# Optimization experiments

Measured on AMD Instinct MI355X. Metric: run time of the kernel, lower is better.

The kernel has to match this reference:

```python
import jax, jax.numpy as jnp
import numpy as np

N = 50000       # nodes
E = 800000      # edges (before self-loops)
G = 512         # graphs in batch
IN = 128        # in_channels
HID = 256       # hidden_channels
HEADS = 8
CH = HID // HEADS
NEG_SLOPE = 0.2 # GATConv leaky relu slope
BN_EPS = 1e-5
OUT_CLASSES = [3, 3]


def setup_inputs() -> dict:
    key = jax.random.key(0)
    ks = iter(jax.random.split(key, 64))
    inp = {}
    inp["x"] = jax.random.normal(next(ks), (N, IN), jnp.float32)
    inp["edge_index"] = jax.random.randint(next(ks), (2, E), 0, N)
    inp["batch"] = jnp.sort(jax.random.randint(next(ks), (N,), 0, G))
    dims = [IN, HID, HID]
    for l, d in enumerate(dims, start=1):
        inp[f"W{l}"] = jax.random.normal(next(ks), (d, HID), jnp.float32) / np.float32(np.sqrt(d))
        inp[f"as{l}"] = jax.random.normal(next(ks), (HEADS, CH), jnp.float32) * 0.1
        inp[f"ad{l}"] = jax.random.normal(next(ks), (HEADS, CH), jnp.float32) * 0.1
        inp[f"b{l}"] = jnp.zeros((HID,), jnp.float32)
        inp[f"g{l}"] = 1.0 + 0.1 * jax.random.normal(next(ks), (HID,), jnp.float32)
        inp[f"be{l}"] = 0.1 * jax.random.normal(next(ks), (HID,), jnp.float32)
        inp[f"m{l}"] = 0.1 * jax.random.normal(next(ks), (HID,), jnp.float32)
        inp[f"v{l}"] = 0.5 + jax.random.uniform(next(ks), (HID,), jnp.float32)
    for i, c in enumerate(OUT_CLASSES):
        inp[f"ow{i}"] = jax.random.normal(next(ks), (3 * HID, c), jnp.float32) / np.float32(np.sqrt(3 * HID))
        inp[f"ob{i}"] = jnp.zeros((c,), jnp.float32)
    return inp


def gat_conv(x, W, a_src, a_dst, bias, src, dst):
    # x: [N, D] -> h: [N, H, C]
    h = (x @ W).reshape(N, HEADS, CH)
    s_src = jnp.sum(h * a_src, axis=-1)           # [N, H]
    s_dst = jnp.sum(h * a_dst, axis=-1)           # [N, H]
    alpha = jax.nn.leaky_relu(s_src[src] + s_dst[dst], NEG_SLOPE)  # [E', H]
    # segment softmax over incoming edges of each destination node
    mx = jax.ops.segment_max(alpha, dst, num_segments=N)           # [N, H]
    e = jnp.exp(alpha - mx[dst])
    Z = jax.ops.segment_sum(e, dst, num_segments=N)                # [N, H]
    coef = e / (Z[dst] + 1e-16)                                    # [E', H]
    msg = h[src] * coef[:, :, None]                                # [E', H, C]
    out = jax.ops.segment_sum(msg, dst, num_segments=N)            # [N, H, C]
    return out.reshape(N, HID) + bias


def batch_norm(h, g, b, m, v):
    return (h - m) * jax.lax.rsqrt(v + BN_EPS) * g + b


def reference(x, edge_index, batch,
              W1, as1, ad1, b1, g1, be1, m1, v1,
              W2, as2, ad2, b2, g2, be2, m2, v2,
              W3, as3, ad3, b3, g3, be3, m3, v3,
              ow0, ob0, ow1, ob1):
    # GATConv adds self-loops by default
    loop = jnp.arange(N, dtype=edge_index.dtype)
    src = jnp.concatenate([edge_index[0], loop])
    dst = jnp.concatenate([edge_index[1], loop])

    h = jax.nn.elu(batch_norm(gat_conv(x, W1, as1, ad1, b1, src, dst), g1, be1, m1, v1))
    h = jax.nn.elu(batch_norm(gat_conv(h, W2, as2, ad2, b2, src, dst), g2, be2, m2, v2) + h)
    h = jax.nn.elu(batch_norm(gat_conv(h, W3, as3, ad3, b3, src, dst), g3, be3, m3, v3) + h)

    sums = jax.ops.segment_sum(h, batch, num_segments=G)                       # add pool
    cnt = jax.ops.segment_sum(jnp.ones((N, 1), h.dtype), batch, num_segments=G)
    mean = sums / jnp.maximum(cnt, 1.0)                                        # mean pool
    mx = jax.ops.segment_max(h, batch, num_segments=G)                         # max pool
    mx = jnp.where(jnp.isfinite(mx), mx, 0.0)
    pooled = jnp.concatenate([mean, sums, mx], axis=1)                         # [G, 3*HID]

    return (pooled @ ow0 + ob0, pooled @ ow1 + ob1)
```

## Files before the change

kernel.cpp:

```cpp
#include <hip/hip_runtime.h>
#include <hip/hip_bf16.h>
#include <math.h>

#define N_NODES 50000
#define N_EDGES 800000
#define EP (N_EDGES + N_NODES)
#define G_GRAPHS 512
#define HID 256
#define HEADS 8
#define NEG_SLOPE 0.2f
#define BN_EPS 1e-5f
#define NB_SCAN ((N_NODES + 1023) / 1024)

typedef __attribute__((ext_vector_type(8))) short short8;
typedef __attribute__((ext_vector_type(8))) unsigned short ushort8v;
typedef __attribute__((ext_vector_type(4))) float floatx4;

__device__ __forceinline__ float bf2f(ushort u) {
    return __uint_as_float(((unsigned)u) << 16);
}
__device__ __forceinline__ ushort f2bf(float f) {
    unsigned u = __float_as_uint(f);
    u += 0x7fff + ((u >> 16) & 1);
    return (ushort)(u >> 16);
}


__global__ void hist_kernel(const int* __restrict__ ei, int* __restrict__ fill) {
    int e = blockIdx.x * 256 + threadIdx.x;
    if (e >= EP) return;
    int d = (e < N_EDGES) ? ei[N_EDGES + e] : (e - N_EDGES);
    atomicAdd(&fill[d], 1);
}

__global__ void scan1_kernel(const int* __restrict__ fill, int* __restrict__ rowptr,
                             int* __restrict__ bsum) {
    __shared__ int sdata[1024];
    int tid = threadIdx.x;
    int idx = blockIdx.x * 1024 + tid;
    int v = (idx < N_NODES) ? fill[idx] : 0;
    sdata[tid] = v;
    __syncthreads();
    for (int off = 1; off < 1024; off <<= 1) {
        int x = (tid >= off) ? sdata[tid - off] : 0;
        __syncthreads();
        sdata[tid] += x;
        __syncthreads();
    }
    if (idx < N_NODES) rowptr[idx] = sdata[tid] - v;
    if (tid == 1023) bsum[blockIdx.x] = sdata[1023];
}

__global__ void scan2_kernel(int* __restrict__ bsum) {
    int lane = threadIdx.x;
    int v = (lane < NB_SCAN) ? bsum[lane] : 0;
    int incl = v;
#pragma unroll
    for (int off = 1; off < 64; off <<= 1) {
        int x = __shfl_up(incl, off, 64);
        if (lane >= off) incl += x;
    }
    if (lane < NB_SCAN) bsum[lane] = incl - v;
    if (lane == NB_SCAN - 1) bsum[NB_SCAN] = incl;
}

__global__ void scan3_kernel(int* __restrict__ rowptr, int* __restrict__ fill,
                             const int* __restrict__ bsum) {
    int idx = blockIdx.x * 1024 + threadIdx.x;
    if (idx < N_NODES) {
        int e = rowptr[idx] + bsum[blockIdx.x];
        rowptr[idx] = e;
        fill[idx] = e;
    }
    if (idx == N_NODES) rowptr[N_NODES] = bsum[NB_SCAN];
}

__global__ void scatter_kernel(const int* __restrict__ ei, int* __restrict__ fill,
                               int* __restrict__ esrc) {
    int e = blockIdx.x * 256 + threadIdx.x;
    if (e >= EP) return;
    int s, d;
    if (e < N_EDGES) { s = ei[e]; d = ei[N_EDGES + e]; }
    else             { s = d = e - N_EDGES; }
    int pos = atomicAdd(&fill[d], 1);
    esrc[pos] = s;
}

__global__ void gstart_kernel(const int* __restrict__ batch, int* __restrict__ gstart) {
    int g = blockIdx.x * 64 + threadIdx.x;
    if (g > G_GRAPHS) return;
    int lo = 0, hi = N_NODES;
    while (lo < hi) { int mid = (lo + hi) >> 1; if (batch[mid] < g) lo = mid + 1; else hi = mid; }
    gstart[g] = lo;
}


__global__ void cvt_kernel(const float* __restrict__ in, ushort* __restrict__ out, int n4) {
    int i = blockIdx.x * 256 + threadIdx.x;
    if (i >= n4) return;
    float4 v = *(const float4*)&in[(size_t)i * 4];
    ushort4 o = {f2bf(v.x), f2bf(v.y), f2bf(v.z), f2bf(v.w)};
    *(ushort4*)&out[(size_t)i * 4] = o;
}

__global__ void wt_all_kernel(const float* __restrict__ W0, const float* __restrict__ W1,
                              const float* __restrict__ W2, ushort* __restrict__ Wt0,
                              ushort* __restrict__ Wt1, ushort* __restrict__ Wt2) {
    int m = blockIdx.y;
    const float* W = (m == 0) ? W0 : (m == 1) ? W1 : W2;
    ushort* Wt = (m == 0) ? Wt0 : (m == 1) ? Wt1 : Wt2;
    int K = (m == 0) ? 128 : 256;
    int c = blockIdx.x, k = threadIdx.x;
    if (k < K) Wt[(size_t)c * K + k] = f2bf(W[(size_t)k * HID + c]);
}

#define BM 128
#define BN 128
#define BK 64

__global__ __launch_bounds__(256) void gemm_kernel(
    const ushort* __restrict__ A, const ushort* __restrict__ Bt,
    ushort* __restrict__ C, int M, int K)
{
    __shared__ __align__(16) char As[BM * BK * 2];
    __shared__ __align__(16) char Bs[BN * BK * 2];

    int t = threadIdx.x;
    int w = t >> 6, lane = t & 63;
    int bm = blockIdx.x * BM, bn = blockIdx.y * BN;
    int wr = (w >> 1) * 64, wc = (w & 1) * 64;

    floatx4 acc[4][4] = {};

    int l8 = lane >> 3;
    int cb = ((lane & 7) << 4) ^ ((l8 & 7) << 4);
    int rsw = (lane & 7) << 4;

    for (int k0 = 0; k0 < K; k0 += BK) {
#pragma unroll
        for (int c = 0; c < 4; c++) {
            int q = w * 4 + c;
            int row = q * 8 + l8;
            int ar = bm + row; if (ar > M - 1) ar = M - 1;
            const char* src = (const char*)A + ((size_t)ar * K + k0) * 2 + cb;
            __builtin_amdgcn_global_load_lds(
                (const __attribute__((address_space(1))) void*)src,
                (__attribute__((address_space(3))) void*)&As[q * 1024], 16, 0, 0);
            int br = bn + row;
            const char* srcb = (const char*)Bt + ((size_t)br * K + k0) * 2 + cb;
            __builtin_amdgcn_global_load_lds(
                (const __attribute__((address_space(1))) void*)srcb,
                (__attribute__((address_space(3))) void*)&Bs[q * 1024], 16, 0, 0);
        }
        __syncthreads();

#pragma unroll
        for (int ks = 0; ks < 2; ks++) {
            int kb = ks * 64 + ((lane >> 4) << 4);
            short8 a[4], b[4];
#pragma unroll
            for (int m = 0; m < 4; m++) {
                int row = wr + m * 16 + (lane & 15);
                a[m] = *(const short8*)&As[row * 128 + (kb ^ rsw)];
            }
#pragma unroll
            for (int n = 0; n < 4; n++) {
                int row = wc + n * 16 + (lane & 15);
                b[n] = *(const short8*)&Bs[row * 128 + (kb ^ rsw)];
            }
#pragma unroll
            for (int m = 0; m < 4; m++)
#pragma unroll
                for (int n = 0; n < 4; n++)
                    acc[m][n] = __builtin_amdgcn_mfma_f32_16x16x32_bf16(a[m], b[n], acc[m][n], 0, 0, 0);
        }
        __syncthreads();
    }

    int cl = lane & 15, rh = lane >> 4;
#pragma unroll
    for (int m = 0; m < 4; m++) {
#pragma unroll
        for (int r = 0; r < 4; r++) {
            int row = bm + wr + m * 16 + rh * 4 + r;
            if (row < M) {
                size_t base = (size_t)row * HID + bn + wc;
#pragma unroll
                for (int n = 0; n < 4; n++)
                    C[base + n * 16 + cl] = f2bf(acc[m][n][r]);
            }
        }
    }
}

__global__ void score_kernel(const ushort* __restrict__ hb,
                             const float* __restrict__ asrc,
                             const float* __restrict__ adst,
                             float* __restrict__ ssrc, float* __restrict__ sdst) {
    int idx = blockIdx.x * 256 + threadIdx.x;
    if (idx >= N_NODES * HEADS) return;
    int n = idx >> 3, h = idx & 7;
    const ushort* hp = &hb[(size_t)n * HID + h * 32];
    const float* ap = &asrc[h * 32];
    const float* dp = &adst[h * 32];
    float s1 = 0.f, s2 = 0.f;
#pragma unroll
    for (int j = 0; j < 32; j++) {
        float v = bf2f(hp[j]);
        s1 += v * ap[j];
        s2 += v * dp[j];
    }
    ssrc[idx] = s1;
    sdst[idx] = s2;
}

__global__ __launch_bounds__(256) void agg_kernel(
    const ushort* __restrict__ hb, const float* __restrict__ ssrc,
    const float* __restrict__ sdst, const int* __restrict__ rowptr,
    const int* __restrict__ esrc, const float* __restrict__ bias,
    const float* __restrict__ gam, const float* __restrict__ bet,
    const float* __restrict__ bmean, const float* __restrict__ bvar,
    const float* __restrict__ resid, float* __restrict__ outh,
    ushort* __restrict__ outb) {
    int wid = threadIdx.x >> 6;
    int lane = threadIdx.x & 63;
    int n = blockIdx.x * 4 + wid;
    if (n >= N_NODES) return;
    int start = rowptr[n], end = rowptr[n + 1];
    int slot = lane >> 5;
    int cl = lane & 31;
    int c0 = cl * 8;
    int head = cl >> 2;
    float sdh = ssrc ? sdst[(size_t)n * 8 + head] : 0.f;

    float z = 0.f;
    float acc[8] = {};
    int i = start + slot;
    for (; i + 2 < end; i += 4) {
        int s0 = esrc[i], s1 = esrc[i + 2];
        float a0 = ssrc[(size_t)s0 * 8 + head] + sdh;
        float a1 = ssrc[(size_t)s1 * 8 + head] + sdh;
        a0 = (a0 >= 0.f) ? a0 : NEG_SLOPE * a0;
        a1 = (a1 >= 0.f) ? a1 : NEG_SLOPE * a1;
        float e0 = __expf(a0);
        float e1 = __expf(a1);
        ushort8v h0 = *(const ushort8v*)&hb[(size_t)s0 * HID + c0];
        ushort8v h1 = *(const ushort8v*)&hb[(size_t)s1 * HID + c0];
        z += e0 + e1;
#pragma unroll
        for (int j = 0; j < 8; j++)
            acc[j] += e0 * bf2f(h0[j]) + e1 * bf2f(h1[j]);
    }
    if (i < end) {
        int s = esrc[i];
        float a = ssrc[(size_t)s * 8 + head] + sdh;
        a = (a >= 0.f) ? a : NEG_SLOPE * a;
        float e = __expf(a);
        ushort8v hv = *(const ushort8v*)&hb[(size_t)s * HID + c0];
        z += e;
#pragma unroll
        for (int j = 0; j < 8; j++)
            acc[j] += e * bf2f(hv[j]);
    }
    z += __shfl_xor(z, 32, 64);
#pragma unroll
    for (int j = 0; j < 8; j++)
        acc[j] += __shfl_xor(acc[j], 32, 64);

    if (lane < 32) {
        float inv = 1.f / (z + 1e-16f);
        float4 bv0 = *(const float4*)&bias[c0],   bv1 = *(const float4*)&bias[c0 + 4];
        float4 gv0 = *(const float4*)&gam[c0],    gv1 = *(const float4*)&gam[c0 + 4];
        float4 be0 = *(const float4*)&bet[c0],    be1 = *(const float4*)&bet[c0 + 4];
        float4 mv0 = *(const float4*)&bmean[c0],  mv1 = *(const float4*)&bmean[c0 + 4];
        float4 vv0 = *(const float4*)&bvar[c0],   vv1 = *(const float4*)&bvar[c0 + 4];
        float bs[8] = {bv0.x, bv0.y, bv0.z, bv0.w, bv1.x, bv1.y, bv1.z, bv1.w};
        float gs[8] = {gv0.x, gv0.y, gv0.z, gv0.w, gv1.x, gv1.y, gv1.z, gv1.w};
        float bes[8] = {be0.x, be0.y, be0.z, be0.w, be1.x, be1.y, be1.z, be1.w};
        float ms[8] = {mv0.x, mv0.y, mv0.z, mv0.w, mv1.x, mv1.y, mv1.z, mv1.w};
        float vs[8] = {vv0.x, vv0.y, vv0.z, vv0.w, vv1.x, vv1.y, vv1.z, vv1.w};
        float rs[8] = {};
        if (resid) {
            float4 r0 = *(const float4*)&resid[(size_t)n * HID + c0];
            float4 r1 = *(const float4*)&resid[(size_t)n * HID + c0 + 4];
            rs[0] = r0.x; rs[1] = r0.y; rs[2] = r0.z; rs[3] = r0.w;
            rs[4] = r1.x; rs[5] = r1.y; rs[6] = r1.z; rs[7] = r1.w;
        }
        float out[8];
#pragma unroll
        for (int j = 0; j < 8; j++) {
            float val = acc[j] * inv + bs[j];
            val = (val - ms[j]) * rsqrtf(vs[j] + BN_EPS) * gs[j] + bes[j];
            val += rs[j];
            val = (val > 0.f) ? val : expm1f(val);
            out[j] = val;
        }
        if (outh) {
            float4 o0 = {out[0], out[1], out[2], out[3]};
            float4 o1 = {out[4], out[5], out[6], out[7]};
            *(float4*)&outh[(size_t)n * HID + c0] = o0;
            *(float4*)&outh[(size_t)n * HID + c0 + 4] = o1;
        }
        if (outb) {
            ushort8v ob;
#pragma unroll
            for (int j = 0; j < 8; j++) ob[j] = f2bf(out[j]);
            *(ushort8v*)&outb[(size_t)n * HID + c0] = ob;
        }
    }
}

__global__ void poolhead_kernel(const ushort* __restrict__ hbf, const int* __restrict__ gstart,
                                const float* __restrict__ ow0, const float* __restrict__ ob0,
                                const float* __restrict__ ow1, const float* __restrict__ ob1,
                                float* __restrict__ out) {
    int g = blockIdx.x;
    int t = threadIdx.x;
    int s = gstart[g], e = gstart[g + 1];
    float sum = 0.f, mx = -INFINITY;
    for (int n = s; n < e; n++) {
        float v = bf2f(hbf[(size_t)n * HID + t]);
        sum += v;
        mx = fmaxf(mx, v);
    }
    int cnt = e - s;
    float mean = sum / fmaxf((float)cnt, 1.f);
    if (cnt == 0) mx = 0.f;

    float a0[3], a1[3];
#pragma unroll
    for (int j = 0; j < 3; j++) {
        a0[j] = mean * ow0[t * 3 + j] + sum * ow0[(256 + t) * 3 + j] + mx * ow0[(512 + t) * 3 + j];
        a1[j] = mean * ow1[t * 3 + j] + sum * ow1[(256 + t) * 3 + j] + mx * ow1[(512 + t) * 3 + j];
    }
    __shared__ float sd[6][256];
#pragma unroll
    for (int j = 0; j < 3; j++) { sd[j][t] = a0[j]; sd[3 + j][t] = a1[j]; }
    __syncthreads();
    for (int off = 128; off; off >>= 1) {
        if (t < off) {
#pragma unroll
            for (int j = 0; j < 6; j++) sd[j][t] += sd[j][t + off];
        }
        __syncthreads();
    }
    if (t < 3) {
        out[g * 3 + t] = sd[t][0] + ob0[t];
        out[1536 + g * 3 + t] = sd[3 + t][0] + ob1[t];
    }
}

extern "C" void kernel_launch(void* const* d_in, const int* in_sizes, int n_in,
                              void* d_out, int out_size, void* d_ws, size_t ws_size,
                              hipStream_t stream) {
    const float* x     = (const float*)d_in[0];
    const int*   ei    = (const int*)d_in[1];
    const int*   batch = (const int*)d_in[2];
    const float* W[3]  = {(const float*)d_in[3], (const float*)d_in[11], (const float*)d_in[19]};
    const float* AS[3] = {(const float*)d_in[4], (const float*)d_in[12], (const float*)d_in[20]};
    const float* AD[3] = {(const float*)d_in[5], (const float*)d_in[13], (const float*)d_in[21]};
    const float* B[3]  = {(const float*)d_in[6], (const float*)d_in[14], (const float*)d_in[22]};
    const float* GM[3] = {(const float*)d_in[7], (const float*)d_in[15], (const float*)d_in[23]};
    const float* BE[3] = {(const float*)d_in[8], (const float*)d_in[16], (const float*)d_in[24]};
    const float* M[3]  = {(const float*)d_in[9], (const float*)d_in[17], (const float*)d_in[25]};
    const float* V[3]  = {(const float*)d_in[10], (const float*)d_in[18], (const float*)d_in[26]};
    const float* ow0 = (const float*)d_in[27];
    const float* ob0 = (const float*)d_in[28];
    const float* ow1 = (const float*)d_in[29];
    const float* ob1 = (const float*)d_in[30];
    float* out = (float*)d_out;

    char* p = (char*)d_ws;
    int* rowptr = (int*)p;  p += (size_t)(N_NODES + 1) * 4;
    int* fill   = (int*)p;  p += (size_t)N_NODES * 4;
    int* esrc   = (int*)p;  p += (size_t)EP * 4;
    int* gstart = (int*)p;  p += (size_t)(G_GRAPHS + 1) * 4;
    int* bsum   = (int*)p;  p += (size_t)(NB_SCAN + 1) * 4;
    p = (char*)(((uintptr_t)p + 255) & ~(uintptr_t)255);
    ushort* hb    = (ushort*)p; p += (size_t)N_NODES * HID * 2;
    float*  curh  = (float*)p;  p += (size_t)N_NODES * HID * 4;
    ushort* curhb = (ushort*)p; p += (size_t)N_NODES * HID * 2;
    ushort* xb    = (ushort*)p; p += (size_t)N_NODES * 128 * 2;
    ushort* Wt0   = (ushort*)p; p += (size_t)256 * 128 * 2;
    ushort* Wt1   = (ushort*)p; p += (size_t)256 * 256 * 2;
    ushort* Wt2   = (ushort*)p; p += (size_t)256 * 256 * 2;
    float* ssrc   = (float*)p;  p += (size_t)N_NODES * HEADS * 4;
    float* sdst   = (float*)p;  p += (size_t)N_NODES * HEADS * 4;

    hipMemsetAsync(fill, 0, (size_t)N_NODES * 4, stream);
    hist_kernel<<<(EP + 255) / 256, 256, 0, stream>>>(ei, fill);
    scan1_kernel<<<NB_SCAN, 1024, 0, stream>>>(fill, rowptr, bsum);
    scan2_kernel<<<1, 64, 0, stream>>>(bsum);
    scan3_kernel<<<NB_SCAN, 1024, 0, stream>>>(rowptr, fill, bsum);
    scatter_kernel<<<(EP + 255) / 256, 256, 0, stream>>>(ei, fill, esrc);
    gstart_kernel<<<(G_GRAPHS + 64) / 64, 64, 0, stream>>>(batch, gstart);

    cvt_kernel<<<(N_NODES * 128 / 4 + 255) / 256, 256, 0, stream>>>(x, xb, N_NODES * 128 / 4);
    {
        dim3 wgrid(256, 3);
        wt_all_kernel<<<wgrid, 256, 0, stream>>>(W[0], W[1], W[2], Wt0, Wt1, Wt2);
    }
    const ushort* Wt[3] = {Wt0, Wt1, Wt2};

    dim3 ggrid((N_NODES + BM - 1) / BM, HID / BN);
    int sgrid = (N_NODES * HEADS + 255) / 256;
    int agrid = (N_NODES + 3) / 4;

    gemm_kernel<<<ggrid, 256, 0, stream>>>(xb, Wt[0], hb, N_NODES, 128);
    score_kernel<<<sgrid, 256, 0, stream>>>(hb, AS[0], AD[0], ssrc, sdst);
    agg_kernel<<<agrid, 256, 0, stream>>>(hb, ssrc, sdst, rowptr, esrc,
                                          B[0], GM[0], BE[0], M[0], V[0],
                                          nullptr, curh, curhb);
    gemm_kernel<<<ggrid, 256, 0, stream>>>(curhb, Wt[1], hb, N_NODES, 256);
    score_kernel<<<sgrid, 256, 0, stream>>>(hb, AS[1], AD[1], ssrc, sdst);
    agg_kernel<<<agrid, 256, 0, stream>>>(hb, ssrc, sdst, rowptr, esrc,
                                          B[1], GM[1], BE[1], M[1], V[1],
                                          curh, curh, curhb);
    gemm_kernel<<<ggrid, 256, 0, stream>>>(curhb, Wt[2], hb, N_NODES, 256);
    score_kernel<<<sgrid, 256, 0, stream>>>(hb, AS[2], AD[2], ssrc, sdst);
    agg_kernel<<<agrid, 256, 0, stream>>>(hb, ssrc, sdst, rowptr, esrc,
                                          B[2], GM[2], BE[2], M[2], V[2],
                                          curh, nullptr, curhb);

    poolhead_kernel<<<G_GRAPHS, 256, 0, stream>>>(curhb, gstart, ow0, ob0, ow1, ob1, out);
}
```

Before: 622.2 us.

## Double-buffer GEMM, fuse scan passes, unroll aggregation, keep residual in bf16

The single-block prefix-scan kernel is folded into scan3, so each block recomputes the block offsets itself and one launch goes away. The GEMM now double-buffers its LDS tiles with explicit vmcnt waits and barriers, so the global loads for the next tile overlap the MFMA work on the current one. The aggregation loop handles four edges per slot per iteration to expose more memory-level parallelism. The fp32 residual/activation buffer is dropped: the residual is read from the bf16 copy and updated in place, which cuts aggregation memory traffic but rounds the residual path to bf16.

```diff
diff --git a/kernel.cpp b/kernel.cpp
--- a/kernel.cpp
+++ b/kernel.cpp
@@ -51,28 +51,29 @@
     if (tid == 1023) bsum[blockIdx.x] = sdata[1023];
 }
 
-__global__ void scan2_kernel(int* __restrict__ bsum) {
-    int lane = threadIdx.x;
-    int v = (lane < NB_SCAN) ? bsum[lane] : 0;
-    int incl = v;
-#pragma unroll
-    for (int off = 1; off < 64; off <<= 1) {
-        int x = __shfl_up(incl, off, 64);
-        if (lane >= off) incl += x;
-    }
-    if (lane < NB_SCAN) bsum[lane] = incl - v;
-    if (lane == NB_SCAN - 1) bsum[NB_SCAN] = incl;
-}
-
 __global__ void scan3_kernel(int* __restrict__ rowptr, int* __restrict__ fill,
                              const int* __restrict__ bsum) {
-    int idx = blockIdx.x * 1024 + threadIdx.x;
+    __shared__ int soff[2];
+    int tid = threadIdx.x;
+    if (tid < 64) {
+        int v = (tid < NB_SCAN) ? bsum[tid] : 0;
+        int incl = v;
+#pragma unroll
+        for (int off = 1; off < 64; off <<= 1) {
+            int x = __shfl_up(incl, off, 64);
+            if (tid >= off) incl += x;
+        }
+        if (tid == blockIdx.x) soff[0] = incl - v;
+        if (tid == NB_SCAN - 1) soff[1] = incl;
+    }
+    __syncthreads();
+    int idx = blockIdx.x * 1024 + tid;
     if (idx < N_NODES) {
-        int e = rowptr[idx] + bsum[blockIdx.x];
+        int e = rowptr[idx] + soff[0];
         rowptr[idx] = e;
         fill[idx] = e;
     }
-    if (idx == N_NODES) rowptr[N_NODES] = bsum[NB_SCAN];
+    if (idx == N_NODES) rowptr[N_NODES] = soff[1];
 }
 
 __global__ void scatter_kernel(const int* __restrict__ ei, int* __restrict__ fill,
@@ -122,8 +123,8 @@
     const ushort* __restrict__ A, const ushort* __restrict__ Bt,
     ushort* __restrict__ C, int M, int K)
 {
-    __shared__ __align__(16) char As[BM * BK * 2];
-    __shared__ __align__(16) char Bs[BN * BK * 2];
+    __shared__ __align__(16) char As[2][BM * BK * 2];
+    __shared__ __align__(16) char Bs[2][BN * BK * 2];
 
     int t = threadIdx.x;
     int w = t >> 6, lane = t & 63;
@@ -135,8 +136,9 @@
     int l8 = lane >> 3;
     int cb = ((lane & 7) << 4) ^ ((l8 & 7) << 4);
     int rsw = (lane & 7) << 4;
-
-    for (int k0 = 0; k0 < K; k0 += BK) {
+    int nt = K / BK;
+
+    auto stage = [&](int buf, int k0) {
 #pragma unroll
         for (int c = 0; c < 4; c++) {
             int q = w * 4 + c;
@@ -145,15 +147,31 @@
             const char* src = (const char*)A + ((size_t)ar * K + k0) * 2 + cb;
             __builtin_amdgcn_global_load_lds(
                 (const __attribute__((address_space(1))) void*)src,
-                (__attribute__((address_space(3))) void*)&As[q * 1024], 16, 0, 0);
+                (__attribute__((address_space(3))) void*)&As[buf][q * 1024], 16, 0, 0);
             int br = bn + row;
             const char* srcb = (const char*)Bt + ((size_t)br * K + k0) * 2 + cb;
             __builtin_amdgcn_global_load_lds(
                 (const __attribute__((address_space(1))) void*)srcb,
-                (__attribute__((address_space(3))) void*)&Bs[q * 1024], 16, 0, 0);
-        }
-        __syncthreads();
-
+                (__attribute__((address_space(3))) void*)&Bs[buf][q * 1024], 16, 0, 0);
+        }
+    };
+
+    stage(0, 0);
+    for (int tt = 0; tt < nt; tt++) {
+        int cur = tt & 1;
+        __builtin_amdgcn_s_barrier();
+        if (tt + 1 < nt) {
+            stage(cur ^ 1, (tt + 1) * BK);
+            asm volatile("s_waitcnt vmcnt(8)" ::: "memory");
+        } else {
+            asm volatile("s_waitcnt vmcnt(0)" ::: "memory");
+        }
+        __builtin_amdgcn_sched_barrier(0);
+        __builtin_amdgcn_s_barrier();
+        __builtin_amdgcn_sched_barrier(0);
+
+        const char* asb = As[cur];
+        const char* bsb = Bs[cur];
 #pragma unroll
         for (int ks = 0; ks < 2; ks++) {
             int kb = ks * 64 + ((lane >> 4) << 4);
@@ -161,12 +179,12 @@
 #pragma unroll
             for (int m = 0; m < 4; m++) {
                 int row = wr + m * 16 + (lane & 15);
-                a[m] = *(const short8*)&As[row * 128 + (kb ^ rsw)];
+                a[m] = *(const short8*)&asb[row * 128 + (kb ^ rsw)];
             }
 #pragma unroll
             for (int n = 0; n < 4; n++) {
                 int row = wc + n * 16 + (lane & 15);
-                b[n] = *(const short8*)&Bs[row * 128 + (kb ^ rsw)];
+                b[n] = *(const short8*)&bsb[row * 128 + (kb ^ rsw)];
             }
 #pragma unroll
             for (int m = 0; m < 4; m++)
@@ -174,7 +192,6 @@
                 for (int n = 0; n < 4; n++)
                     acc[m][n] = __builtin_amdgcn_mfma_f32_16x16x32_bf16(a[m], b[n], acc[m][n], 0, 0, 0);
         }
-        __syncthreads();
     }
 
     int cl = lane & 15, rh = lane >> 4;
@@ -220,8 +237,7 @@
     const int* __restrict__ esrc, const float* __restrict__ bias,
     const float* __restrict__ gam, const float* __restrict__ bet,
     const float* __restrict__ bmean, const float* __restrict__ bvar,
-    const float* __restrict__ resid, float* __restrict__ outh,
-    ushort* __restrict__ outb) {
+    const ushort* __restrict__ residb, ushort* __restrict__ outb) {
     int wid = threadIdx.x >> 6;
     int lane = threadIdx.x & 63;
     int n = blockIdx.x * 4 + wid;
@@ -231,27 +247,33 @@
     int cl = lane & 31;
     int c0 = cl * 8;
     int head = cl >> 2;
-    float sdh = ssrc ? sdst[(size_t)n * 8 + head] : 0.f;
+    float sdh = sdst[(size_t)n * 8 + head];
 
     float z = 0.f;
     float acc[8] = {};
     int i = start + slot;
-    for (; i + 2 < end; i += 4) {
-        int s0 = esrc[i], s1 = esrc[i + 2];
+    for (; i + 6 < end; i += 8) {
+        int s0 = esrc[i], s1 = esrc[i + 2], s2 = esrc[i + 4], s3 = esrc[i + 6];
         float a0 = ssrc[(size_t)s0 * 8 + head] + sdh;
         float a1 = ssrc[(size_t)s1 * 8 + head] + sdh;
+        float a2 = ssrc[(size_t)s2 * 8 + head] + sdh;
+        float a3 = ssrc[(size_t)s3 * 8 + head] + sdh;
+        ushort8v h0 = *(const ushort8v*)&hb[(size_t)s0 * HID + c0];
+        ushort8v h1 = *(const ushort8v*)&hb[(size_t)s1 * HID + c0];
+        ushort8v h2 = *(const ushort8v*)&hb[(size_t)s2 * HID + c0];
+        ushort8v h3 = *(const ushort8v*)&hb[(size_t)s3 * HID + c0];
         a0 = (a0 >= 0.f) ? a0 : NEG_SLOPE * a0;
         a1 = (a1 >= 0.f) ? a1 : NEG_SLOPE * a1;
-        float e0 = __expf(a0);
-        float e1 = __expf(a1);
-        ushort8v h0 = *(const ushort8v*)&hb[(size_t)s0 * HID + c0];
-        ushort8v h1 = *(const ushort8v*)&hb[(size_t)s1 * HID + c0];
-        z += e0 + e1;
+        a2 = (a2 >= 0.f) ? a2 : NEG_SLOPE * a2;
+        a3 = (a3 >= 0.f) ? a3 : NEG_SLOPE * a3;
+        float e0 = __expf(a0), e1 = __expf(a1), e2 = __expf(a2), e3 = __expf(a3);
+        z += (e0 + e1) + (e2 + e3);
 #pragma unroll
         for (int j = 0; j < 8; j++)
-            acc[j] += e0 * bf2f(h0[j]) + e1 * bf2f(h1[j]);
-    }
-    if (i < end) {
+            acc[j] += (e0 * bf2f(h0[j]) + e1 * bf2f(h1[j])) +
+                      (e2 * bf2f(h2[j]) + e3 * bf2f(h3[j]));
+    }
+    for (; i < end; i += 2) {
         int s = esrc[i];
         float a = ssrc[(size_t)s * 8 + head] + sdh;
         a = (a >= 0.f) ? a : NEG_SLOPE * a;
@@ -280,33 +302,21 @@
         float ms[8] = {mv0.x, mv0.y, mv0.z, mv0.w, mv1.x, mv1.y, mv1.z, mv1.w};
         float vs[8] = {vv0.x, vv0.y, vv0.z, vv0.w, vv1.x, vv1.y, vv1.z, vv1.w};
         float rs[8] = {};
-        if (resid) {
-            float4 r0 = *(const float4*)&resid[(size_t)n * HID + c0];
-            float4 r1 = *(const float4*)&resid[(size_t)n * HID + c0 + 4];
-            rs[0] = r0.x; rs[1] = r0.y; rs[2] = r0.z; rs[3] = r0.w;
-            rs[4] = r1.x; rs[5] = r1.y; rs[6] = r1.z; rs[7] = r1.w;
-        }
-        float out[8];
+        if (residb) {
+            ushort8v rv = *(const ushort8v*)&residb[(size_t)n * HID + c0];
+#pragma unroll
+            for (int j = 0; j < 8; j++) rs[j] = bf2f(rv[j]);
+        }
+        ushort8v ob;
 #pragma unroll
         for (int j = 0; j < 8; j++) {
             float val = acc[j] * inv + bs[j];
             val = (val - ms[j]) * rsqrtf(vs[j] + BN_EPS) * gs[j] + bes[j];
             val += rs[j];
             val = (val > 0.f) ? val : expm1f(val);
-            out[j] = val;
-        }
-        if (outh) {
-            float4 o0 = {out[0], out[1], out[2], out[3]};
-            float4 o1 = {out[4], out[5], out[6], out[7]};
-            *(float4*)&outh[(size_t)n * HID + c0] = o0;
-            *(float4*)&outh[(size_t)n * HID + c0 + 4] = o1;
-        }
-        if (outb) {
-            ushort8v ob;
-#pragma unroll
-            for (int j = 0; j < 8; j++) ob[j] = f2bf(out[j]);
-            *(ushort8v*)&outb[(size_t)n * HID + c0] = ob;
-        }
+            ob[j] = f2bf(val);
+        }
+        *(ushort8v*)&outb[(size_t)n * HID + c0] = ob;
     }
 }
 
@@ -378,7 +388,6 @@
     int* bsum   = (int*)p;  p += (size_t)(NB_SCAN + 1) * 4;
     p = (char*)(((uintptr_t)p + 255) & ~(uintptr_t)255);
     ushort* hb    = (ushort*)p; p += (size_t)N_NODES * HID * 2;
-    float*  curh  = (float*)p;  p += (size_t)N_NODES * HID * 4;
     ushort* curhb = (ushort*)p; p += (size_t)N_NODES * HID * 2;
     ushort* xb    = (ushort*)p; p += (size_t)N_NODES * 128 * 2;
     ushort* Wt0   = (ushort*)p; p += (size_t)256 * 128 * 2;
@@ -390,7 +399,6 @@
     hipMemsetAsync(fill, 0, (size_t)N_NODES * 4, stream);
     hist_kernel<<<(EP + 255) / 256, 256, 0, stream>>>(ei, fill);
     scan1_kernel<<<NB_SCAN, 1024, 0, stream>>>(fill, rowptr, bsum);
-    scan2_kernel<<<1, 64, 0, stream>>>(bsum);
     scan3_kernel<<<NB_SCAN, 1024, 0, stream>>>(rowptr, fill, bsum);
     scatter_kernel<<<(EP + 255) / 256, 256, 0, stream>>>(ei, fill, esrc);
     gstart_kernel<<<(G_GRAPHS + 64) / 64, 64, 0, stream>>>(batch, gstart);
@@ -410,17 +418,14 @@
     score_kernel<<<sgrid, 256, 0, stream>>>(hb, AS[0], AD[0], ssrc, sdst);
     agg_kernel<<<agrid, 256, 0, stream>>>(hb, ssrc, sdst, rowptr, esrc,
                                           B[0], GM[0], BE[0], M[0], V[0],
-                                          nullptr, curh, curhb);
-    gemm_kernel<<<ggrid, 256, 0, stream>>>(curhb, Wt[1], hb, N_NODES, 256);
-    score_kernel<<<sgrid, 256, 0, stream>>>(hb, AS[1], AD[1], ssrc, sdst);
-    agg_kernel<<<agrid, 256, 0, stream>>>(hb, ssrc, sdst, rowptr, esrc,
-                                          B[1], GM[1], BE[1], M[1], V[1],
-                                          curh, curh, curhb);
-    gemm_kernel<<<ggrid, 256, 0, stream>>>(curhb, Wt[2], hb, N_NODES, 256);
-    score_kernel<<<sgrid, 256, 0, stream>>>(hb, AS[2], AD[2], ssrc, sdst);
-    agg_kernel<<<agrid, 256, 0, stream>>>(hb, ssrc, sdst, rowptr, esrc,
-                                          B[2], GM[2], BE[2], M[2], V[2],
-                                          curh, nullptr, curhb);
+                                          nullptr, curhb);
+    for (int l = 1; l < 3; l++) {
+        gemm_kernel<<<ggrid, 256, 0, stream>>>(curhb, Wt[l], hb, N_NODES, 256);
+        score_kernel<<<sgrid, 256, 0, stream>>>(hb, AS[l], AD[l], ssrc, sdst);
+        agg_kernel<<<agrid, 256, 0, stream>>>(hb, ssrc, sdst, rowptr, esrc,
+                                              B[l], GM[l], BE[l], M[l], V[l],
+                                              curhb, curhb);
+    }
 
     poolhead_kernel<<<G_GRAPHS, 256, 0, stream>>>(curhb, gstart, ow0, ob0, ow1, ob1, out);
 }
```

After: 599.7 us. 1.04x faster.
